# Performance work log

Measured on AMD Instinct MI355X. Metric: run time of the kernel, lower is better.

The kernel has to match this reference:

```python
import jax, jax.numpy as jnp
import numpy as np

K = 20           # neighbors
ALPHA = 1.0      # clustering alpha
BN_EPS = 1e-5
NEG_SLOPE = 0.2


def knn_idx(x, k):
    # x: (B, C, N) -> idx (B, N, k) of k nearest neighbors by squared L2
    xx = jnp.sum(x * x, axis=1)                      # (B, N)
    inner = jnp.einsum('bcn,bcm->bnm', x, x)         # (B, N, N)
    pd = -xx[:, :, None] + 2.0 * inner - xx[:, None, :]  # negative sq dist
    return jax.lax.top_k(pd, k)[1]


def graph_feature(x, k):
    # x: (B, C, N) -> (B, 2C, N, k): concat(neighbor - center, center)
    xt = jnp.transpose(x, (0, 2, 1))                 # (B, N, C)
    idx = knn_idx(x, k)                              # (B, N, k)
    feat = jax.vmap(lambda f, i: f[i])(xt, idx)      # (B, N, k, C)
    center = jnp.broadcast_to(xt[:, :, None, :], feat.shape)
    out = jnp.concatenate([feat - center, center], axis=-1)
    return jnp.transpose(out, (0, 3, 1, 2))


def batchnorm(x, g, b, axes):
    # training-mode BN: batch statistics over `axes`, channel axis = 1
    m = jnp.mean(x, axes, keepdims=True)
    v = jnp.var(x, axes, keepdims=True)
    shape = [1] * x.ndim
    shape[1] = x.shape[1]
    return (x - m) / jnp.sqrt(v + BN_EPS) * g.reshape(shape) + b.reshape(shape)


def conv_block2d(x, w, g, b):
    # 1x1 Conv2d (no bias) + BN2d + LeakyReLU; x (B,Cin,N,k), w (Cout,Cin)
    y = jnp.einsum('oc,bcnk->bonk', w, x)
    return jax.nn.leaky_relu(batchnorm(y, g, b, (0, 2, 3)), NEG_SLOPE)


def setup_inputs() -> dict:
    key = jax.random.key(0)
    ks = jax.random.split(key, 16)
    B, C, N = 4, 3, 2048
    d = {
        'x1': jax.random.normal(ks[0], (B, C, N), jnp.float32),
        'x2': jax.random.normal(ks[1], (B, C, N), jnp.float32),
        'w1': jax.random.normal(ks[2], (64, 6), jnp.float32) * 0.1,
        'g1': jnp.ones((64,), jnp.float32), 'b1': jnp.zeros((64,), jnp.float32),
        'w2': jax.random.normal(ks[3], (64, 128), jnp.float32) * 0.1,
        'g2': jnp.ones((64,), jnp.float32), 'b2': jnp.zeros((64,), jnp.float32),
        'w3': jax.random.normal(ks[4], (128, 128), jnp.float32) * 0.1,
        'g3': jnp.ones((128,), jnp.float32), 'b3': jnp.zeros((128,), jnp.float32),
        'w4': jax.random.normal(ks[5], (256, 256), jnp.float32) * 0.1,
        'g4': jnp.ones((256,), jnp.float32), 'b4': jnp.zeros((256,), jnp.float32),
        'w5': jax.random.normal(ks[6], (1024, 512), jnp.float32) * 0.05,
        'g5': jnp.ones((1024,), jnp.float32), 'b5': jnp.zeros((1024,), jnp.float32),
        'lw1': jax.random.normal(ks[7], (256, 2048), jnp.float32) * 0.02,
        'lb1': jnp.zeros((256,), jnp.float32),
        'lw2': jax.random.normal(ks[8], (64, 256), jnp.float32) * 0.05,
        'lb2': jnp.zeros((64,), jnp.float32),
        'lw3': jax.random.normal(ks[9], (10, 64), jnp.float32) * 0.1,
        'lb3': jnp.zeros((10,), jnp.float32),
        'cw': jax.random.normal(ks[10], (800, 10), jnp.float32) * 0.1,
    }
    return d


def reference(x1, x2, w1, g1, b1, w2, g2, b2, w3, g3, b3, w4, g4, b4,
              w5, g5, b5, lw1, lb1, lw2, lb2, lw3, lb3, cw):

    def single(x):
        h = conv_block2d(graph_feature(x, K), w1, g1, b1)
        f1 = h.max(axis=-1)                            # (B,64,N)
        h = conv_block2d(graph_feature(f1, K), w2, g2, b2)
        f2 = h.max(axis=-1)                            # (B,64,N)
        h = conv_block2d(graph_feature(f2, K), w3, g3, b3)
        f3 = h.max(axis=-1)                            # (B,128,N)
        h = conv_block2d(graph_feature(f3, K), w4, g4, b4)
        f4 = h.max(axis=-1)                            # (B,256,N)
        h = jnp.concatenate([f1, f2, f3, f4], axis=1)  # (B,512,N)
        h = jnp.einsum('oc,bcn->bon', w5, h)           # 1x1 Conv1d
        h = jax.nn.leaky_relu(batchnorm(h, g5, b5, (0, 2)), NEG_SLOPE)
        z = jnp.concatenate([h.max(axis=-1), h.mean(axis=-1)], axis=1)  # (B,2048)
        z = z @ lw1.T + lb1
        z = z @ lw2.T + lb2
        e = z @ lw3.T + lb3                            # (B,10)
        diff = e[:, None, :] - cw                      # (B,800,10)
        x_dis = jnp.sum(diff * diff, axis=2)           # (B,800)
        q = (1.0 + x_dis / ALPHA) ** (-(ALPHA + 1.0) / 2.0)
        q = q / jnp.sum(q, axis=1, keepdims=True)
        return q, e, x_dis

    q1, e1, xd1 = single(x1)
    q2, e2, xd2 = single(x2)
    d = e1 - e2 + 1e-6  # torch F.pairwise_distance eps
    sim = jnp.sqrt(jnp.sum(d * d, axis=1))
    return (sim, q1, q2, e1, e2, xd1)
```

## Files before the change

kernel.cpp:

```cpp
#include <hip/hip_runtime.h>
#include <math.h>

#define BB 4
#define NN 2048
#define KK 20
#define NEG 0.2f

#define QOFF0 4
#define QOFF1 3204
#define EOFF0 6404
#define EOFF1 6444
#define XDOFF 6484

typedef unsigned short u16;
typedef unsigned int u32;
typedef __attribute__((ext_vector_type(8))) short s16x8;
typedef __attribute__((ext_vector_type(16))) float f32x16;
typedef __attribute__((ext_vector_type(8))) u16 u16x8;

__global__ __launch_bounds__(256) void transpose_x_kernel(
    const float* __restrict__ x, float* __restrict__ fnc, float* __restrict__ xx)
{
    int gid = blockIdx.x * 256 + threadIdx.x;
    int b = gid >> 11, n = gid & 2047;
    float s = 0.f;
#pragma unroll
    for (int c = 0; c < 3; ++c) {
        float v = x[((size_t)b * 3 + c) * NN + n];
        fnc[(size_t)gid * 3 + c] = v;
        s += v * v;
    }
    xx[gid] = s;
}

__global__ __launch_bounds__(256) void norms_kernel(
    const float* __restrict__ h512, int choff, int C, float* __restrict__ xx)
{
    int gid = blockIdx.x * 256 + threadIdx.x;
    const float* p = h512 + (size_t)gid * 512 + choff;
    float s = 0.f;
    for (int c = 0; c < C; ++c) { float v = p[c]; s += v * v; }
    xx[gid] = s;
}

template<int CTRL>
__device__ __forceinline__ void dpp_step(float& v, int& i)
{
    int vi = __float_as_int(v);
    int nv = __builtin_amdgcn_update_dpp(vi, vi, CTRL, 0xf, 0xf, false);
    int ni = __builtin_amdgcn_update_dpp(i,  i,  CTRL, 0xf, 0xf, false);
    float nvf = __int_as_float(nv);
    if (nvf > v || (nvf == v && ni < i)) { v = nvf; i = ni; }
}

template<int C>
__global__ __launch_bounds__(512, 4) void knn_kernel(
    const float* __restrict__ fcn,
    const float* __restrict__ fnc,
    int ncs, int choff,
    const float* __restrict__ xx, int* __restrict__ idxout)
{
    __shared__ float sbuf[8][NN];
    int tid = threadIdx.x;
    int bid = blockIdx.x;
    int b   = bid & 3;
    int n0  = (((bid >> 3) << 1) | ((bid >> 2) & 1)) * 8;

    const float* fb = fcn + (size_t)b * C * NN;
    const float* xb = xx + b * NN;
    const float* cbase = fnc + (size_t)(b * NN + n0) * ncs + choff;

    float a0[8], a1[8], a2[8], a3[8];
#pragma unroll
    for (int r = 0; r < 8; ++r) { a0[r] = 0.f; a1[r] = 0.f; a2[r] = 0.f; a3[r] = 0.f; }

    const float* fp = fb + 4 * tid;

    if constexpr (C % 4 == 0) {
        float4 buf[4];
#pragma unroll
        for (int q = 0; q < 4; ++q) buf[q] = *(const float4*)(fp + (size_t)q * NN);
        for (int cg = 0; cg < C; cg += 4) {
            float4 nxt[4];
            if (cg + 4 < C) {
#pragma unroll
                for (int q = 0; q < 4; ++q)
                    nxt[q] = *(const float4*)(fp + (size_t)(cg + 4 + q) * NN);
            } else {
#pragma unroll
                for (int q = 0; q < 4; ++q) nxt[q] = buf[q];
            }
            float4 cv[8];
#pragma unroll
            for (int r = 0; r < 8; ++r)
                cv[r] = *(const float4*)(cbase + (size_t)r * ncs + cg);
#pragma unroll
            for (int r = 0; r < 8; ++r) {
                a0[r] += cv[r].x * buf[0].x; a1[r] += cv[r].x * buf[0].y;
                a2[r] += cv[r].x * buf[0].z; a3[r] += cv[r].x * buf[0].w;
                a0[r] += cv[r].y * buf[1].x; a1[r] += cv[r].y * buf[1].y;
                a2[r] += cv[r].y * buf[1].z; a3[r] += cv[r].y * buf[1].w;
                a0[r] += cv[r].z * buf[2].x; a1[r] += cv[r].z * buf[2].y;
                a2[r] += cv[r].z * buf[2].z; a3[r] += cv[r].z * buf[2].w;
                a0[r] += cv[r].w * buf[3].x; a1[r] += cv[r].w * buf[3].y;
                a2[r] += cv[r].w * buf[3].z; a3[r] += cv[r].w * buf[3].w;
            }
#pragma unroll
            for (int q = 0; q < 4; ++q) buf[q] = nxt[q];
        }
    } else {
        for (int c = 0; c < C; ++c) {
            float cr[8];
#pragma unroll
            for (int r = 0; r < 8; ++r) cr[r] = cbase[(size_t)r * ncs + c];
            float4 v = *(const float4*)(fp + (size_t)c * NN);
#pragma unroll
            for (int r = 0; r < 8; ++r) {
                a0[r] += cr[r] * v.x; a1[r] += cr[r] * v.y;
                a2[r] += cr[r] * v.z; a3[r] += cr[r] * v.w;
            }
        }
    }
    {
        float4 xm = *(const float4*)(xb + 4 * tid);
#pragma unroll
        for (int r = 0; r < 8; ++r) {
            float4 sv = {2.f * a0[r] - xm.x, 2.f * a1[r] - xm.y,
                         2.f * a2[r] - xm.z, 2.f * a3[r] - xm.w};
            *(float4*)&sbuf[r][4 * tid] = sv;
        }
    }
    __syncthreads();

    int w = tid >> 6, lane = tid & 63;
    float* sb = sbuf[w];
    int* op = idxout + (size_t)(b * NN + n0 + w) * KK;
    const float NINF = -3.4e38f;

    float rv[32];
#pragma unroll
    for (int j = 0; j < 32; ++j) rv[j] = sb[lane + (j << 6)];

    unsigned consumed = 0u;

    float v1 = NINF, v2 = NINF; int j1 = -1, j2 = -1;
#pragma unroll
    for (int j = 0; j < 32; ++j) {
        float vv = rv[j];
        if (vv > v1) { v2 = v1; j2 = j1; v1 = vv; j1 = j; }
        else if (vv > v2) { v2 = vv; j2 = j; }
    }
    int i1 = (j1 < 0) ? -1 : lane + (j1 << 6);
    int i2 = (j2 < 0) ? -1 : lane + (j2 << 6);

    for (int it = 0; it < KK; ++it) {
        float bv = v1; int bi = i1;
        dpp_step<0x111>(bv, bi);
        dpp_step<0x112>(bv, bi);
        dpp_step<0x114>(bv, bi);
        dpp_step<0x118>(bv, bi);
        dpp_step<0x142>(bv, bi);
        dpp_step<0x143>(bv, bi);
        int win = __builtin_amdgcn_readlane(bi, 63);
        if (lane == 0) op[it] = win;
        if (i1 == win) {
            consumed |= 1u << j1;
            v1 = v2; i1 = i2; j1 = j2;
            v2 = NINF; i2 = -1; j2 = -1;
        }
        if (__any(v1 == NINF)) {
            if (v1 == NINF) {
                v1 = NINF; v2 = NINF; j1 = -1; j2 = -1;
#pragma unroll
                for (int j = 0; j < 32; ++j) {
                    if (!(consumed & (1u << j))) {
                        float vv = rv[j];
                        if (vv > v1) { v2 = v1; j2 = j1; v1 = vv; j1 = j; }
                        else if (vv > v2) { v2 = vv; j2 = j; }
                    }
                }
                i1 = (j1 < 0) ? -1 : lane + (j1 << 6);
                i2 = (j2 < 0) ? -1 : lane + (j2 << 6);
            }
        }
    }
}

template<int C, int COUT>
__global__ __launch_bounds__(256) void gemm_gh_kernel(
    const float* __restrict__ fnc, int ncs, int choff,
    const float* __restrict__ W,
    float* __restrict__ G, float* __restrict__ H)
{
    constexpr int GROUPS = 256 / COUT;
    constexpr int RPT = 8 / GROUPS;
    __shared__ float Fs[8][C];
    int tid = threadIdx.x;
    int row0 = blockIdx.x * 8;
    for (int i = tid; i < 8 * C; i += 256) {
        int r = i / C, c = i % C;
        Fs[r][c] = fnc[(size_t)(row0 + r) * ncs + choff + c];
    }
    __syncthreads();
    int o = tid % COUT;
    int r0 = (tid / COUT) * RPT;
    float g[RPT], h[RPT];
#pragma unroll
    for (int r = 0; r < RPT; ++r) { g[r] = 0.f; h[r] = 0.f; }
    const float* wr = W + (size_t)o * 2 * C;
    for (int c = 0; c < C; ++c) {
        float w1 = wr[c], wd = wr[C + c] - w1;
#pragma unroll
        for (int r = 0; r < RPT; ++r) {
            float f = Fs[r0 + r][c];
            g[r] += f * w1; h[r] += f * wd;
        }
    }
#pragma unroll
    for (int r = 0; r < RPT; ++r) {
        size_t rr = (size_t)(row0 + r0 + r) * COUT + o;
        G[rr] = g[r]; H[rr] = h[r];
    }
}

template<int COUT>
__global__ __launch_bounds__(256) void gather_kernel(
    const float* __restrict__ G, const float* __restrict__ H,
    const int* __restrict__ idx,
    float* __restrict__ ymax, float* __restrict__ ymin,
    float* __restrict__ psum, float* __restrict__ psumsq)
{
    constexpr int RPI = 256 / COUT;
    constexpr int NITER = 16 / RPI;
    int tid = threadIdx.x;
    int o = tid % COUT;
    int rsub = tid / COUT;
    int row0 = blockIdx.x * 16;
    float s = 0.f, s2 = 0.f;
    for (int it = 0; it < NITER; ++it) {
        int r = row0 + it * RPI + rsub;
        int b = r >> 11;
        float h = H[(size_t)r * COUT + o];
        const int* ip = idx + (size_t)r * KK;
        float mx = -3.4e38f, mn = 3.4e38f;
#pragma unroll
        for (int j = 0; j < KK; ++j) {
            int m = ip[j];
            float g = G[((size_t)(b << 11) + m) * COUT + o];
            float y = g + h;
            mx = fmaxf(mx, y); mn = fminf(mn, y);
            s += y; s2 += y * y;
        }
        ymax[(size_t)r * COUT + o] = mx;
        ymin[(size_t)r * COUT + o] = mn;
    }
    __shared__ float ls[256], ls2[256];
    ls[tid] = s; ls2[tid] = s2;
    __syncthreads();
    for (int st = 128; st >= COUT; st >>= 1) {
        if (tid < st) { ls[tid] += ls[tid + st]; ls2[tid] += ls2[tid + st]; }
        __syncthreads();
    }
    if (tid < COUT) {
        psum[(size_t)blockIdx.x * COUT + tid]   = ls[tid];
        psumsq[(size_t)blockIdx.x * COUT + tid] = ls2[tid];
    }
}

__global__ __launch_bounds__(256) void bnscale_kernel(
    const float* __restrict__ psum, const float* __restrict__ psumsq,
    int nblk, int cout, float cnt,
    const float* __restrict__ gw, const float* __restrict__ bw,
    float* __restrict__ ss)
{
    int o = blockIdx.x;
    int t = threadIdx.x;
    float s = 0.f, s2 = 0.f;
    for (int i = t; i < nblk; i += 256) {
        s  += psum[(size_t)i * cout + o];
        s2 += psumsq[(size_t)i * cout + o];
    }
    __shared__ float ls[256], ls2[256];
    ls[t] = s; ls2[t] = s2;
    __syncthreads();
    for (int st = 128; st > 0; st >>= 1) {
        if (t < st) { ls[t] += ls[t + st]; ls2[t] += ls2[t + st]; }
        __syncthreads();
    }
    if (t == 0) {
        float m = ls[0] / cnt;
        float v = ls2[0] / cnt - m * m;
        float sc = gw[o] / sqrtf(v + 1e-5f);
        float sh = bw[o] - m * sc;
        ss[o * 2] = sc; ss[o * 2 + 1] = sh;
    }
}

__global__ __launch_bounds__(256) void apply_kernel(
    const float* __restrict__ ymax, const float* __restrict__ ymin,
    const float* __restrict__ ss, int coutShift, int choff,
    float* __restrict__ h512)
{
    size_t gid = (size_t)blockIdx.x * 256 + threadIdx.x;
    int o = (int)(gid & ((1u << coutShift) - 1));
    size_t r = gid >> coutShift;
    float sc = ss[o * 2], sh = ss[o * 2 + 1];
    float v = (sc >= 0.f) ? ymax[gid] : ymin[gid];
    float a = sc * v + sh;
    float act = (a > 0.f) ? a : NEG * a;
    h512[r * 512 + choff + o] = act;
}

template<int CO>
__global__ __launch_bounds__(256) void apply_t_kernel(
    const float* __restrict__ ymax, const float* __restrict__ ymin,
    const float* __restrict__ ss, int choff,
    float* __restrict__ h512, float* __restrict__ fcn)
{
    constexpr int TILES_O = CO >> 6;
    __shared__ float tile[64][65];
    int tr = blockIdx.x / TILES_O;
    int to = blockIdx.x % TILES_O;
    int r0 = tr * 64, o0 = to * 64;
    int t = threadIdx.x;
    int lr = t >> 6;
    int lo = t & 63;
    int o = o0 + lo;
    float sc = ss[o * 2], sh = ss[o * 2 + 1];
#pragma unroll
    for (int rr = 0; rr < 64; rr += 4) {
        int r = r0 + rr + lr;
        size_t gid = (size_t)r * CO + o;
        float v = (sc >= 0.f) ? ymax[gid] : ymin[gid];
        float a = sc * v + sh;
        float act = (a > 0.f) ? a : NEG * a;
        h512[(size_t)r * 512 + choff + o] = act;
        tile[rr + lr][lo] = act;
    }
    __syncthreads();
    int b = r0 >> 11;
    int n0 = r0 & 2047;
#pragma unroll
    for (int oo = 0; oo < 64; oo += 4) {
        fcn[((size_t)(b * CO + o0 + oo + lr)) * NN + n0 + lo] = tile[lo][oo + lr];
    }
}

__device__ __forceinline__ u16 f2bf(float x) {
    u32 u = __float_as_uint(x);
    u += 0x7FFFu + ((u >> 16) & 1u);
    return (u16)(u >> 16);
}

__global__ __launch_bounds__(256) void tobf16_kernel(
    const float* __restrict__ A, const float* __restrict__ Bm,
    u16* __restrict__ Ah, u16* __restrict__ Al,
    u16* __restrict__ Bh, u16* __restrict__ Bl)
{
    int gid = blockIdx.x * 256 + threadIdx.x;
    const float* src; u16 *dh, *dl; size_t off;
    if (gid < 524288) { src = A;  dh = Ah; dl = Al; off = (size_t)gid * 8; }
    else             { src = Bm; dh = Bh; dl = Bl; off = (size_t)(gid - 524288) * 8; }
    float4 v0 = *(const float4*)(src + off);
    float4 v1 = *(const float4*)(src + off + 4);
    float x[8] = {v0.x, v0.y, v0.z, v0.w, v1.x, v1.y, v1.z, v1.w};
    u16x8 h, l;
#pragma unroll
    for (int j = 0; j < 8; ++j) {
        u16 hb = f2bf(x[j]);
        h[j] = hb;
        l[j] = f2bf(x[j] - __uint_as_float((u32)hb << 16));
    }
    *(u16x8*)(dh + off) = h;
    *(u16x8*)(dl + off) = l;
}

__device__ __forceinline__ void gload_lds16(const void* g, void* l) {
    __builtin_amdgcn_global_load_lds(
        (const __attribute__((address_space(1))) void*)g,
        (__attribute__((address_space(3))) void*)l, 16, 0, 0);
}

__global__ __launch_bounds__(256) void gemm5_mfma_kernel(
    const u16* __restrict__ Ah, const u16* __restrict__ Al,
    const u16* __restrict__ Bh, const u16* __restrict__ Bl,
    float* __restrict__ Y, float* __restrict__ psum, float* __restrict__ psumsq)
{
    __shared__ u16 As[2][128][64];
    __shared__ u16 Bs[2][128][64];
    __shared__ float scs[4][128];
    __shared__ float sqs[4][128];

    int tid = threadIdx.x;
    int bm = blockIdx.x & 63, bn = blockIdx.x >> 6;
    int row0 = bm * 128, col0 = bn * 128;
    int w = tid >> 6, lane = tid & 63;
    int wr = w >> 1, wc = w & 1;

    int isB = w >> 1, plane = w & 1;
    int srow = lane >> 3;
    int kch  = (lane & 7) ^ srow;
    const u16* gbase = isB ? (plane ? Bl : Bh) : (plane ? Al : Ah);
    int rc0 = isB ? col0 : row0;
    const u16* gsrc0 = gbase + (size_t)(rc0 + srow) * 512 + kch * 8;
    u16* lds0 = (isB ? &Bs[0][0][0] : &As[0][0][0]) + plane * 8192;

    f32x16 acc[2][2];
#pragma unroll
    for (int i = 0; i < 2; ++i)
#pragma unroll
        for (int j = 0; j < 2; ++j)
#pragma unroll
            for (int r = 0; r < 16; ++r) acc[i][j][r] = 0.f;

    int ln = lane & 31, l5 = lane >> 5;
    const u16* Afb = &As[0][0][0] + (size_t)(wr * 64 + ln) * 64;
    const u16* Bfb = &Bs[0][0][0] + (size_t)(wc * 64 + ln) * 64;

    for (int k0 = 0; k0 < 512; k0 += 64) {
#pragma unroll
        for (int cc = 0; cc < 16; ++cc)
            gload_lds16(gsrc0 + (size_t)cc * 4096 + k0, lds0 + cc * 512);
        __syncthreads();

#pragma unroll
        for (int ks = 0; ks < 4; ++ks) {
            int pos = ((ks * 2 + l5) ^ (ln & 7)) * 8;
            s16x8 ah0 = *(const s16x8*)(Afb + pos);
            s16x8 ah1 = *(const s16x8*)(Afb + 2048 + pos);
            s16x8 al0 = *(const s16x8*)(Afb + 8192 + pos);
            s16x8 al1 = *(const s16x8*)(Afb + 8192 + 2048 + pos);
#pragma unroll
            for (int j = 0; j < 2; ++j) {
                s16x8 bh = *(const s16x8*)(Bfb + j * 2048 + pos);
                s16x8 bl = *(const s16x8*)(Bfb + 8192 + j * 2048 + pos);
                acc[0][j] = __builtin_amdgcn_mfma_f32_32x32x16_bf16(ah0, bh, acc[0][j], 0, 0, 0);
                acc[1][j] = __builtin_amdgcn_mfma_f32_32x32x16_bf16(ah1, bh, acc[1][j], 0, 0, 0);
                acc[0][j] = __builtin_amdgcn_mfma_f32_32x32x16_bf16(al0, bh, acc[0][j], 0, 0, 0);
                acc[1][j] = __builtin_amdgcn_mfma_f32_32x32x16_bf16(al1, bh, acc[1][j], 0, 0, 0);
                acc[0][j] = __builtin_amdgcn_mfma_f32_32x32x16_bf16(ah0, bl, acc[0][j], 0, 0, 0);
                acc[1][j] = __builtin_amdgcn_mfma_f32_32x32x16_bf16(ah1, bl, acc[1][j], 0, 0, 0);
            }
        }
        __syncthreads();
    }

#pragma unroll
    for (int i = 0; i < 2; ++i)
#pragma unroll
        for (int reg = 0; reg < 16; ++reg) {
            int row = row0 + wr * 64 + i * 32 + l5 * 4 + (reg >> 2) * 8 + (reg & 3);
            float* yp = Y + (size_t)row * 1024 + col0 + wc * 64 + ln;
            yp[0]  = acc[i][0][reg];
            yp[32] = acc[i][1][reg];
        }

#pragma unroll
    for (int j = 0; j < 2; ++j) {
        float s = 0.f, q = 0.f;
#pragma unroll
        for (int i = 0; i < 2; ++i)
#pragma unroll
            for (int reg = 0; reg < 16; ++reg) {
                float v = acc[i][j][reg];
                s += v; q += v * v;
            }
        scs[wr * 2 + l5][wc * 64 + j * 32 + ln] = s;
        sqs[wr * 2 + l5][wc * 64 + j * 32 + ln] = q;
    }
    __syncthreads();
    if (tid < 128) {
        float s = 0.f, q = 0.f;
#pragma unroll
        for (int p = 0; p < 4; ++p) { s += scs[p][tid]; q += sqs[p][tid]; }
        psum[(size_t)bm * 1024 + col0 + tid]   = s;
        psumsq[(size_t)bm * 1024 + col0 + tid] = q;
    }
}

__global__ __launch_bounds__(256) void pool_part_kernel(
    const float* __restrict__ Y, const float* __restrict__ ss,
    float* __restrict__ pmax, float* __restrict__ psum)
{
    int bid = blockIdx.x;
    int b = bid >> 6;
    int n0 = (bid & 63) * 32;
    int t = threadIdx.x;
    int o = t * 4;
    float4 sA = *(const float4*)(ss + o * 2);
    float4 sB = *(const float4*)(ss + o * 2 + 4);
    float4 mx = {-3.4e38f, -3.4e38f, -3.4e38f, -3.4e38f};
    float4 sm = {0.f, 0.f, 0.f, 0.f};
    const float* Yb = Y + ((size_t)b * NN + n0) * 1024 + o;
#pragma unroll 4
    for (int n = 0; n < 32; ++n) {
        float4 v = *(const float4*)(Yb + (size_t)n * 1024);
        float a0 = sA.x * v.x + sA.y; a0 = (a0 > 0.f) ? a0 : NEG * a0;
        float a1 = sA.z * v.y + sA.w; a1 = (a1 > 0.f) ? a1 : NEG * a1;
        float a2 = sB.x * v.z + sB.y; a2 = (a2 > 0.f) ? a2 : NEG * a2;
        float a3 = sB.z * v.w + sB.w; a3 = (a3 > 0.f) ? a3 : NEG * a3;
        mx.x = fmaxf(mx.x, a0); sm.x += a0;
        mx.y = fmaxf(mx.y, a1); sm.y += a1;
        mx.z = fmaxf(mx.z, a2); sm.z += a2;
        mx.w = fmaxf(mx.w, a3); sm.w += a3;
    }
    size_t po = (size_t)bid * 1024 + o;
    *(float4*)(pmax + po) = mx;
    *(float4*)(psum + po) = sm;
}

__global__ __launch_bounds__(256) void pool_comb_kernel(
    const float* __restrict__ pmax, const float* __restrict__ psum,
    float* __restrict__ z)
{
    int b = blockIdx.x;
    int t = threadIdx.x;
    int o = t * 4;
    float4 mx = {-3.4e38f, -3.4e38f, -3.4e38f, -3.4e38f};
    float4 sm = {0.f, 0.f, 0.f, 0.f};
    for (int ch = 0; ch < 64; ++ch) {
        size_t po = ((size_t)(b * 64 + ch)) * 1024 + o;
        float4 m = *(const float4*)(pmax + po);
        float4 s = *(const float4*)(psum + po);
        mx.x = fmaxf(mx.x, m.x); mx.y = fmaxf(mx.y, m.y);
        mx.z = fmaxf(mx.z, m.z); mx.w = fmaxf(mx.w, m.w);
        sm.x += s.x; sm.y += s.y; sm.z += s.z; sm.w += s.w;
    }
    *(float4*)(z + (size_t)b * 2048 + o) = mx;
    float4 mn = {sm.x * (1.f / 2048.f), sm.y * (1.f / 2048.f),
                 sm.z * (1.f / 2048.f), sm.w * (1.f / 2048.f)};
    *(float4*)(z + (size_t)b * 2048 + 1024 + o) = mn;
}

__global__ __launch_bounds__(64) void gemv1_kernel(
    const float* __restrict__ z, const float* __restrict__ lw1,
    const float* __restrict__ lb1, float* __restrict__ z1)
{
    int o = blockIdx.x;
    int lane = threadIdx.x;
    const float* wr = lw1 + (size_t)o * 2048;
    float a0 = 0.f, a1 = 0.f, a2 = 0.f, a3 = 0.f;
    for (int c = lane; c < 2048; c += 64) {
        float w = wr[c];
        a0 += z[c] * w; a1 += z[2048 + c] * w;
        a2 += z[4096 + c] * w; a3 += z[6144 + c] * w;
    }
#pragma unroll
    for (int off = 32; off > 0; off >>= 1) {
        a0 += __shfl_down(a0, off); a1 += __shfl_down(a1, off);
        a2 += __shfl_down(a2, off); a3 += __shfl_down(a3, off);
    }
    if (lane == 0) {
        float bias = lb1[o];
        z1[o] = a0 + bias; z1[256 + o] = a1 + bias;
        z1[512 + o] = a2 + bias; z1[768 + o] = a3 + bias;
    }
}

__global__ __launch_bounds__(1024) void head2_kernel(
    const float* __restrict__ z1,
    const float* __restrict__ lw2, const float* __restrict__ lb2,
    const float* __restrict__ lw3, const float* __restrict__ lb3,
    const float* __restrict__ cw,
    float* __restrict__ out, float* __restrict__ e_store, int which)
{
    __shared__ float z2s[4][64];
    __shared__ float es[4][10];
    __shared__ float qs[3200];
    __shared__ float dnm[4];
    int t = threadIdx.x;
    if (t < 256) {
        int b = t >> 6, o = t & 63;
        float acc = lb2[o];
        const float* wr = lw2 + (size_t)o * 256;
        const float* zr = z1 + b * 256;
        for (int c = 0; c < 256; ++c) acc += zr[c] * wr[c];
        z2s[b][o] = acc;
    }
    __syncthreads();
    if (t < 40) {
        int b = t / 10, o = t % 10;
        float acc = lb3[o];
        const float* wr = lw3 + o * 64;
        for (int c = 0; c < 64; ++c) acc += z2s[b][c] * wr[c];
        es[b][o] = acc;
        int eoff = (which == 0) ? EOFF0 : EOFF1;
        out[eoff + b * 10 + o] = acc;
        e_store[which * 40 + b * 10 + o] = acc;
    }
    __syncthreads();
    for (int p = t; p < 3200; p += 1024) {
        int b = p / 800, j = p % 800;
        float xd = 0.f;
        const float* cwr = cw + j * 10;
#pragma unroll
        for (int i = 0; i < 10; ++i) { float d = es[b][i] - cwr[i]; xd += d * d; }
        qs[p] = 1.0f / (1.0f + xd);
        if (which == 0) out[XDOFF + p] = xd;
    }
    __syncthreads();
    if (t < 4) {
        float s = 0.f;
        for (int j = 0; j < 800; ++j) s += qs[t * 800 + j];
        dnm[t] = s;
    }
    __syncthreads();
    int qoff = (which == 0) ? QOFF0 : QOFF1;
    for (int p = t; p < 3200; p += 1024) out[qoff + p] = qs[p] / dnm[p / 800];
}

__global__ void sim_kernel(const float* __restrict__ e_store, float* __restrict__ out)
{
    int t = threadIdx.x;
    if (t < 4) {
        float s = 0.f;
        for (int i = 0; i < 10; ++i) {
            float d = e_store[t * 10 + i] - e_store[40 + t * 10 + i] + 1e-6f;
            s += d * d;
        }
        out[t] = sqrtf(s);
    }
}

extern "C" void kernel_launch(void* const* d_in, const int* in_sizes, int n_in,
                              void* d_out, int out_size, void* d_ws, size_t ws_size,
                              hipStream_t stream)
{
    const float* x1  = (const float*)d_in[0];
    const float* x2  = (const float*)d_in[1];
    const float* w1  = (const float*)d_in[2];
    const float* g1  = (const float*)d_in[3];
    const float* b1  = (const float*)d_in[4];
    const float* w2  = (const float*)d_in[5];
    const float* g2  = (const float*)d_in[6];
    const float* b2  = (const float*)d_in[7];
    const float* w3  = (const float*)d_in[8];
    const float* g3  = (const float*)d_in[9];
    const float* b3  = (const float*)d_in[10];
    const float* w4  = (const float*)d_in[11];
    const float* g4  = (const float*)d_in[12];
    const float* b4  = (const float*)d_in[13];
    const float* w5  = (const float*)d_in[14];
    const float* g5  = (const float*)d_in[15];
    const float* b5  = (const float*)d_in[16];
    const float* lw1 = (const float*)d_in[17];
    const float* lb1 = (const float*)d_in[18];
    const float* lw2 = (const float*)d_in[19];
    const float* lb2 = (const float*)d_in[20];
    const float* lw3 = (const float*)d_in[21];
    const float* lb3 = (const float*)d_in[22];
    const float* cw  = (const float*)d_in[23];
    float* out = (float*)d_out;

    float* ws   = (float*)d_ws;
    float* h512 = ws;
    float* G    = h512 + 4194304;
    float* Hb   = G + 2097152;
    float* ymax = Hb + 2097152;
    float* ymin = ymax + 2097152;
    float* y5   = G;
    float* fcn  = ymin + 2097152;
    float* fnc1 = fcn + 1048576;
    float* xx   = fnc1 + 32768;
    float* psum = xx + 8192;
    float* psq  = psum + 131072;
    float* ss   = psq + 131072;
    float* p5s  = ss + 2048;
    float* p5q  = p5s + 262144;
    float* ss5  = p5q + 262144;
    float* z    = ss5 + 2048;
    float* z1   = z + 8192;
    float* est  = z1 + 1024;
    int*   idx  = (int*)(est + 128);
    u16*   Ahs  = (u16*)(idx + BB * NN * KK);
    u16*   Als  = Ahs + 4194304;
    u16*   Bhs  = Als + 4194304;
    u16*   Bls  = Bhs + 524288;

    for (int which = 0; which < 2; ++which) {
        const float* xin = which ? x2 : x1;
        transpose_x_kernel<<<32, 256, 0, stream>>>(xin, fnc1, xx);
        knn_kernel<3><<<1024, 512, 0, stream>>>(xin, fnc1, 3, 0, xx, idx);
        gemm_gh_kernel<3, 64><<<1024, 256, 0, stream>>>(fnc1, 3, 0, w1, G, Hb);
        gather_kernel<64><<<512, 256, 0, stream>>>(G, Hb, idx, ymax, ymin, psum, psq);
        bnscale_kernel<<<64, 256, 0, stream>>>(psum, psq, 512, 64, 163840.f, g1, b1, ss);
        apply_t_kernel<64><<<128, 256, 0, stream>>>(ymax, ymin, ss, 0, h512, fcn);
        norms_kernel<<<32, 256, 0, stream>>>(h512, 0, 64, xx);
        knn_kernel<64><<<1024, 512, 0, stream>>>(fcn, h512, 512, 0, xx, idx);
        gemm_gh_kernel<64, 64><<<1024, 256, 0, stream>>>(h512, 512, 0, w2, G, Hb);
        gather_kernel<64><<<512, 256, 0, stream>>>(G, Hb, idx, ymax, ymin, psum, psq);
        bnscale_kernel<<<64, 256, 0, stream>>>(psum, psq, 512, 64, 163840.f, g2, b2, ss);
        apply_t_kernel<64><<<128, 256, 0, stream>>>(ymax, ymin, ss, 64, h512, fcn);
        norms_kernel<<<32, 256, 0, stream>>>(h512, 64, 64, xx);
        knn_kernel<64><<<1024, 512, 0, stream>>>(fcn, h512, 512, 64, xx, idx);
        gemm_gh_kernel<64, 128><<<1024, 256, 0, stream>>>(h512, 512, 64, w3, G, Hb);
        gather_kernel<128><<<512, 256, 0, stream>>>(G, Hb, idx, ymax, ymin, psum, psq);
        bnscale_kernel<<<128, 256, 0, stream>>>(psum, psq, 512, 128, 163840.f, g3, b3, ss);
        apply_t_kernel<128><<<256, 256, 0, stream>>>(ymax, ymin, ss, 128, h512, fcn);
        norms_kernel<<<32, 256, 0, stream>>>(h512, 128, 128, xx);
        knn_kernel<128><<<1024, 512, 0, stream>>>(fcn, h512, 512, 128, xx, idx);
        gemm_gh_kernel<128, 256><<<1024, 256, 0, stream>>>(h512, 512, 128, w4, G, Hb);
        gather_kernel<256><<<512, 256, 0, stream>>>(G, Hb, idx, ymax, ymin, psum, psq);
        bnscale_kernel<<<256, 256, 0, stream>>>(psum, psq, 512, 256, 163840.f, g4, b4, ss);
        apply_kernel<<<8192, 256, 0, stream>>>(ymax, ymin, ss, 8, 256, h512);
        tobf16_kernel<<<2304, 256, 0, stream>>>(h512, w5, Ahs, Als, Bhs, Bls);
        gemm5_mfma_kernel<<<512, 256, 0, stream>>>(Ahs, Als, Bhs, Bls, y5, p5s, p5q);
        bnscale_kernel<<<1024, 256, 0, stream>>>(p5s, p5q, 64, 1024, 8192.f, g5, b5, ss5);
        pool_part_kernel<<<256, 256, 0, stream>>>(y5, ss5, p5s, p5q);
        pool_comb_kernel<<<4, 256, 0, stream>>>(p5s, p5q, z);
        gemv1_kernel<<<256, 64, 0, stream>>>(z, lw1, lb1, z1);
        head2_kernel<<<1, 1024, 0, stream>>>(z1, lw2, lb2, lw3, lb3, cw, out, est, which);
    }
    sim_kernel<<<1, 64, 0, stream>>>(est, out);
}
```

Baseline: 1.330 ms.

## Split fused kNN into dot-product and top-k selection kernels via global scratch

The fused kNN kernel, which computed distance rows into a 64KB shared-memory buffer and then ran top-k selection, is split into two kernels. A dot kernel writes score rows to a global scratch buffer (aliased onto G), two batches at a time, and a separate select kernel with 256-thread blocks reads each row and does the top-k. This frees shared memory and raises the occupancy target of the dot phase (launch bounds 512,8). The cost is a 32MB global write and read of scores per half-batch, plus four extra launches per kNN stage.

```diff
diff --git a/kernel.cpp b/kernel.cpp
--- a/kernel.cpp
+++ b/kernel.cpp
@@ -54,17 +54,18 @@
 }
 
 template<int C>
-__global__ __launch_bounds__(512, 4) void knn_kernel(
+__global__ __launch_bounds__(512, 8) void knn_dot_kernel(
     const float* __restrict__ fcn,
     const float* __restrict__ fnc,
-    int ncs, int choff,
-    const float* __restrict__ xx, int* __restrict__ idxout)
-{
-    __shared__ float sbuf[8][NN];
+    int ncs, int choff, int bbase,
+    const float* __restrict__ xx,
+    float* __restrict__ S)
+{
     int tid = threadIdx.x;
     int bid = blockIdx.x;
-    int b   = bid & 3;
-    int n0  = (((bid >> 3) << 1) | ((bid >> 2) & 1)) * 8;
+    int bl  = bid & 1;
+    int b   = bbase + bl;
+    int n0  = (bid >> 1) * 8;
 
     const float* fb = fcn + (size_t)b * C * NN;
     const float* xb = xx + b * NN;
@@ -127,14 +128,20 @@
         for (int r = 0; r < 8; ++r) {
             float4 sv = {2.f * a0[r] - xm.x, 2.f * a1[r] - xm.y,
                          2.f * a2[r] - xm.z, 2.f * a3[r] - xm.w};
-            *(float4*)&sbuf[r][4 * tid] = sv;
-        }
-    }
-    __syncthreads();
-
+            *(float4*)&S[((size_t)bl * NN + n0 + r) * NN + 4 * tid] = sv;
+        }
+    }
+}
+
+__global__ __launch_bounds__(256) void knn_select_kernel(
+    const float* __restrict__ S, int bbase, int* __restrict__ idxout)
+{
+    int tid = threadIdx.x;
     int w = tid >> 6, lane = tid & 63;
-    float* sb = sbuf[w];
-    int* op = idxout + (size_t)(b * NN + n0 + w) * KK;
+    int row = blockIdx.x * 4 + w;
+    int bl = row >> 11, n = row & 2047;
+    const float* sb = S + ((size_t)bl * NN + n) * NN;
+    int* op = idxout + ((size_t)((bbase + bl) * NN + n)) * KK;
     const float NINF = -3.4e38f;
 
     float rv[32];
@@ -659,6 +666,7 @@
     float* ymax = Hb + 2097152;
     float* ymin = ymax + 2097152;
     float* y5   = G;
+    float* Sscr = G;
     float* fcn  = ymin + 2097152;
     float* fnc1 = fcn + 1048576;
     float* xx   = fnc1 + 32768;
@@ -680,25 +688,37 @@
     for (int which = 0; which < 2; ++which) {
         const float* xin = which ? x2 : x1;
         transpose_x_kernel<<<32, 256, 0, stream>>>(xin, fnc1, xx);
-        knn_kernel<3><<<1024, 512, 0, stream>>>(xin, fnc1, 3, 0, xx, idx);
+        knn_dot_kernel<3><<<512, 512, 0, stream>>>(xin, fnc1, 3, 0, 0, xx, Sscr);
+        knn_select_kernel<<<1024, 256, 0, stream>>>(Sscr, 0, idx);
+        knn_dot_kernel<3><<<512, 512, 0, stream>>>(xin, fnc1, 3, 0, 2, xx, Sscr);
+        knn_select_kernel<<<1024, 256, 0, stream>>>(Sscr, 2, idx);
         gemm_gh_kernel<3, 64><<<1024, 256, 0, stream>>>(fnc1, 3, 0, w1, G, Hb);
         gather_kernel<64><<<512, 256, 0, stream>>>(G, Hb, idx, ymax, ymin, psum, psq);
         bnscale_kernel<<<64, 256, 0, stream>>>(psum, psq, 512, 64, 163840.f, g1, b1, ss);
         apply_t_kernel<64><<<128, 256, 0, stream>>>(ymax, ymin, ss, 0, h512, fcn);
         norms_kernel<<<32, 256, 0, stream>>>(h512, 0, 64, xx);
-        knn_kernel<64><<<1024, 512, 0, stream>>>(fcn, h512, 512, 0, xx, idx);
+        knn_dot_kernel<64><<<512, 512, 0, stream>>>(fcn, h512, 512, 0, 0, xx, Sscr);
+        knn_select_kernel<<<1024, 256, 0, stream>>>(Sscr, 0, idx);
+        knn_dot_kernel<64><<<512, 512, 0, stream>>>(fcn, h512, 512, 0, 2, xx, Sscr);
+        knn_select_kernel<<<1024, 256, 0, stream>>>(Sscr, 2, idx);
         gemm_gh_kernel<64, 64><<<1024, 256, 0, stream>>>(h512, 512, 0, w2, G, Hb);
         gather_kernel<64><<<512, 256, 0, stream>>>(G, Hb, idx, ymax, ymin, psum, psq);
         bnscale_kernel<<<64, 256, 0, stream>>>(psum, psq, 512, 64, 163840.f, g2, b2, ss);
         apply_t_kernel<64><<<128, 256, 0, stream>>>(ymax, ymin, ss, 64, h512, fcn);
         norms_kernel<<<32, 256, 0, stream>>>(h512, 64, 64, xx);
-        knn_kernel<64><<<1024, 512, 0, stream>>>(fcn, h512, 512, 64, xx, idx);
+        knn_dot_kernel<64><<<512, 512, 0, stream>>>(fcn, h512, 512, 64, 0, xx, Sscr);
+        knn_select_kernel<<<1024, 256, 0, stream>>>(Sscr, 0, idx);
+        knn_dot_kernel<64><<<512, 512, 0, stream>>>(fcn, h512, 512, 64, 2, xx, Sscr);
+        knn_select_kernel<<<1024, 256, 0, stream>>>(Sscr, 2, idx);
         gemm_gh_kernel<64, 128><<<1024, 256, 0, stream>>>(h512, 512, 64, w3, G, Hb);
         gather_kernel<128><<<512, 256, 0, stream>>>(G, Hb, idx, ymax, ymin, psum, psq);
         bnscale_kernel<<<128, 256, 0, stream>>>(psum, psq, 512, 128, 163840.f, g3, b3, ss);
         apply_t_kernel<128><<<256, 256, 0, stream>>>(ymax, ymin, ss, 128, h512, fcn);
         norms_kernel<<<32, 256, 0, stream>>>(h512, 128, 128, xx);
-        knn_kernel<128><<<1024, 512, 0, stream>>>(fcn, h512, 512, 128, xx, idx);
+        knn_dot_kernel<128><<<512, 512, 0, stream>>>(fcn, h512, 512, 128, 0, xx, Sscr);
+        knn_select_kernel<<<1024, 256, 0, stream>>>(Sscr, 0, idx);
+        knn_dot_kernel<128><<<512, 512, 0, stream>>>(fcn, h512, 512, 128, 2, xx, Sscr);
+        knn_select_kernel<<<1024, 256, 0, stream>>>(Sscr, 2, idx);
         gemm_gh_kernel<128, 256><<<1024, 256, 0, stream>>>(h512, 512, 128, w4, G, Hb);
         gather_kernel<256><<<512, 256, 0, stream>>>(G, Hb, idx, ymax, ymin, psum, psq);
         bnscale_kernel<<<256, 256, 0, stream>>>(psum, psq, 512, 256, 163840.f, g4, b4, ss);
```

After: 1.762 ms. 32.5% more time.
